# Performance work log

Measured on AMD Instinct MI355X. Metric: run time of the kernel, lower is better.

Reference implementation:

```python
import jax, jax.numpy as jnp
import numpy as np


def _round_ste(v):
    # straight-through rounding (typical LinearQuantize autograd STE)
    return v + jax.lax.stop_gradient(jnp.round(v) - v)


def setup_inputs() -> dict:
    key = jax.random.key(0)
    k1, k2, k3 = jax.random.split(key, 3)
    tokens, d_in, d_out = 8192, 2048, 2048
    x = jax.random.uniform(k1, (tokens, d_in), dtype=jnp.float32)  # non-negative acts
    weight = jax.random.normal(k2, (d_out, d_in), dtype=jnp.float32) * 0.02
    bias = jax.random.normal(k3, (d_out,), dtype=jnp.float32) * 0.02
    return {"x": x, "weight": weight, "bias": bias, "weight_bit": 8}


def reference(x, weight, bias, weight_bit):
    n = 2 ** weight_bit
    # stats computed on detached data (x.data/w.data in torch)
    wd = jax.lax.stop_gradient(weight)
    w_min = wd.min(axis=1)                      # [out]
    w_max = wd.max(axis=1)                      # [out]
    x_max = jax.lax.stop_gradient(x).max()
    scale_x = (n - 1) / jnp.clip(x_max, 1e-8)
    # activation quantization: round(scale_x * x - 0)
    q_x = _round_ste(scale_x * x)               # [T, in]
    # per-channel asymmetric weight quant (quantize_int)
    scale_w = (n - 1) / jnp.clip(w_max - w_min, 1e-8)   # [out]
    zp_w = scale_w * w_min                      # [out]
    q_w = _round_ste(scale_w[:, None] * weight - zp_w[:, None])  # [out, in]
    # bias quantized with combined scale, then clamped
    q_b = jnp.clip(_round_ste(bias * scale_w * scale_x), -n - 1, n)  # [out]
    # fake-int GEMM + zero-point correction + rescale
    mult = jnp.einsum('ti,oi->to', q_x, q_w) + q_b      # [T, out]
    res = mult + zp_w * q_x.sum(-1, keepdims=True)
    return res / scale_x / scale_w
```

## Files before the change

### kernel.cpp

```cpp
#include <hip/hip_runtime.h>
#include <stdint.h>

typedef __attribute__((ext_vector_type(4))) int i32x4;

__device__ inline float wave_max(float v){ for(int o=32;o;o>>=1) v=fmaxf(v,__shfl_xor(v,o)); return v; }
__device__ inline float wave_min(float v){ for(int o=32;o;o>>=1) v=fminf(v,__shfl_xor(v,o)); return v; }
__device__ inline int   wave_sum(int v){ for(int o=32;o;o>>=1) v+=__shfl_xor(v,o); return v; }

__device__ inline void gload16(const void* g, void* l){
  __builtin_amdgcn_global_load_lds((const __attribute__((address_space(1))) char*)g,
                                   (__attribute__((address_space(3))) char*)l, 16, 0, 0);
}

__global__ void k_xmax_partial(const float* __restrict__ x, long long n4,
                               float* __restrict__ partials){
  long long i = (long long)blockIdx.x*blockDim.x + threadIdx.x;
  long long stride = (long long)gridDim.x*blockDim.x;
  const float4* x4 = (const float4*)x;
  float m = 0.f;
  for(; i < n4; i += stride){
    float4 v = x4[i];
    m = fmaxf(m, fmaxf(fmaxf(v.x,v.y),fmaxf(v.z,v.w)));
  }
  m = wave_max(m);
  __shared__ float sm[4];
  int lane = threadIdx.x & 63, wid = threadIdx.x >> 6;
  if(lane==0) sm[wid] = m;
  __syncthreads();
  if(threadIdx.x==0)
    partials[blockIdx.x] = fmaxf(fmaxf(sm[0],sm[1]),fmaxf(sm[2],sm[3]));
}

__global__ void k_xmax_final(const float* __restrict__ partials, int nPart,
                             uint32_t* __restrict__ xmax_bits){
  float m = 0.f;
  for(int i = threadIdx.x; i < nPart; i += 256) m = fmaxf(m, partials[i]);
  m = wave_max(m);
  __shared__ float sm[4];
  int lane = threadIdx.x & 63, wid = threadIdx.x >> 6;
  if(lane==0) sm[wid] = m;
  __syncthreads();
  if(threadIdx.x==0)
    *xmax_bits = __float_as_uint(fmaxf(fmaxf(sm[0],sm[1]),fmaxf(sm[2],sm[3])));
}

__global__ void k_wstat(const float* __restrict__ w,
                        const int* __restrict__ wbit,
                        float* __restrict__ scale_w, float* __restrict__ zp_w,
                        float* __restrict__ winv,
                        int* __restrict__ cint, char* __restrict__ qw, int din){
  int row = blockIdx.x, tid = threadIdx.x;
  int lane = tid & 63, wid = tid >> 6;
  const float4* wr4 = (const float4*)(w + (long long)row*din);
  float4 a = wr4[tid*2], b = wr4[tid*2+1];
  float v[8] = {a.x,a.y,a.z,a.w,b.x,b.y,b.z,b.w};
  float mn = v[0], mx = v[0];
  for(int j=1;j<8;j++){ mn=fminf(mn,v[j]); mx=fmaxf(mx,v[j]); }
  float wmn = wave_min(mn), wmx = wave_max(mx);
  __shared__ float smn[4], smx[4];
  __shared__ float s_sw, s_zp;
  if(lane==0){ smn[wid]=wmn; smx[wid]=wmx; }
  __syncthreads();
  if(tid==0){
    float fmn = fminf(fminf(smn[0],smn[1]),fminf(smn[2],smn[3]));
    float fmx = fmaxf(fmaxf(smx[0],smx[1]),fmaxf(smx[2],smx[3]));
    int n = 1 << *wbit;
    float nm1 = (float)(n-1);
    float rngc = fmaxf(__fsub_rn(fmx, fmn), 1e-8f);
    float sw = __fdiv_rn(nm1, rngc);
    float zp = __fmul_rn(sw, fmn);
    s_sw = sw; s_zp = zp;
    scale_w[row] = sw; zp_w[row] = zp;
    winv[row] = __fdiv_rn(rngc, nm1);
  }
  __syncthreads();
  float sw = s_sw, zp = s_zp;
  int qsum = 0; uint32_t lo = 0, hi = 0;
  for(int j=0;j<8;j++){
    int q = (int)rintf(__fsub_rn(__fmul_rn(sw, v[j]), zp));
    qsum += q;
    uint32_t u = (uint32_t)((q - 128) & 0xff);
    if(j<4) lo |= u << (8*j); else hi |= u << (8*(j-4));
  }
  uint32_t* qrow = (uint32_t*)(qw + (long long)row*din);
  qrow[tid*2] = lo; qrow[tid*2+1] = hi;
  int wsum = wave_sum(qsum);
  __shared__ int ssum[4];
  if(lane==0) ssum[wid] = wsum;
  __syncthreads();
  if(tid==0){
    int Sb = ssum[0]+ssum[1]+ssum[2]+ssum[3];
    cint[row] = 128*Sb - 128*128*din;
  }
}

__global__ void k_xquant(const float* __restrict__ x, const int* __restrict__ wbit,
                         const uint32_t* __restrict__ xmax_bits,
                         char* __restrict__ qx, int* __restrict__ Sa, int din){
  int row = blockIdx.x, tid = threadIdx.x;
  int lane = tid & 63, wid = tid >> 6;
  int n = 1 << *wbit;
  float nm1 = (float)(n-1);
  float sx = __fdiv_rn(nm1, fmaxf(__uint_as_float(*xmax_bits), 1e-8f));
  const float4* xr4 = (const float4*)(x + (long long)row*din);
  float4 a = xr4[tid*2], b = xr4[tid*2+1];
  float v[8] = {a.x,a.y,a.z,a.w,b.x,b.y,b.z,b.w};
  int qsum = 0; uint32_t lo = 0, hi = 0;
  for(int j=0;j<8;j++){
    int q = (int)rintf(__fmul_rn(sx, v[j]));
    qsum += q;
    uint32_t u = (uint32_t)((q - 128) & 0xff);
    if(j<4) lo |= u << (8*j); else hi |= u << (8*(j-4));
  }
  uint32_t* qrow = (uint32_t*)(qx + (long long)row*din);
  qrow[tid*2] = lo; qrow[tid*2+1] = hi;
  int wsum = wave_sum(qsum);
  __shared__ int ssum[4];
  if(lane==0) ssum[wid] = wsum;
  __syncthreads();
  if(tid==0) Sa[row] = ssum[0]+ssum[1]+ssum[2]+ssum[3];
}

__global__ __launch_bounds__(512, 2) void k_gemm(
    const char* __restrict__ qx, const char* __restrict__ qw,
    const int* __restrict__ Sa, const int* __restrict__ cint,
    const float* __restrict__ scale_w, const float* __restrict__ winv,
    const float* __restrict__ zp_w, const float* __restrict__ bias,
    const int* __restrict__ wbit, const uint32_t* __restrict__ xmax_bits,
    float* __restrict__ out, int T, int dout, int din){
  extern __shared__ char lds[];
  const int tid = threadIdx.x, lane = tid & 63, wid = tid >> 6;
  const int wr = wid >> 2, wc = wid & 3;
  const int tileN = blockIdx.x, tileM = blockIdx.y;
  const int nt = din / 128;

  const int i0 = tid, i1 = tid + 512;
  const int r0 = i0 >> 2, r1 = i1 >> 2;
  const int sc0 = ((i0 & 3) ^ ((r0 >> 1) & 3)) * 16;
  const int sc1 = ((i1 & 3) ^ ((r1 >> 1) & 3)) * 16;
  const char* aS0 = qx + ((long long)tileM*256 + r0)*din + sc0;
  const char* aS1 = qx + ((long long)tileM*256 + r1)*din + sc1;
  const char* bS0 = qw + ((long long)tileN*256 + r0)*din + sc0;
  const char* bS1 = qw + ((long long)tileN*256 + r1)*din + sc1;
  const int d0 = i0*16, d1 = i1*16;

  const int physo = (((lane >> 4) ^ ((lane >> 1) & 3)) * 16);
  const int arowL = wr*128 + (lane & 15);
  const int browL = wc*64  + (lane & 15);

  i32x4 acc[8][4] = {};
  i32x4 af[4], bf[4];

#define STAGE_A(KS, KOFF, NB) do{ \
    gload16(aS0 + (KOFF) + (KS)*64, (NB) + (KS)*16384 + d0); \
    gload16(aS1 + (KOFF) + (KS)*64, (NB) + (KS)*16384 + d1); }while(0)
#define STAGE_B(KS, KOFF, NB) do{ \
    gload16(bS0 + (KOFF) + (KS)*64, (NB) + 32768 + (KS)*16384 + d0); \
    gload16(bS1 + (KOFF) + (KS)*64, (NB) + 32768 + (KS)*16384 + d1); }while(0)

  STAGE_A(0, 0, lds); STAGE_B(0, 0, lds);
  STAGE_A(1, 0, lds); STAGE_B(1, 0, lds);
  asm volatile("s_waitcnt vmcnt(4)" ::: "memory");
  __builtin_amdgcn_s_barrier();

  for(int t = 0; t < nt; ++t){
    char* Ab = lds + (t & 1)*65536;
    char* Bb = Ab + 32768;
    char* NB = lds + ((t & 1)^1)*65536;
    const bool ld = (t + 1 < nt);
    const int koff = (t + 1)*128;

#define PH(MH, KS, DO_B, STAGE_STMT, VM_STMT) do{ \
    if(DO_B){ _Pragma("unroll") \
      for(int ni=0;ni<4;++ni) bf[ni] = *(const i32x4*)(Bb + (KS)*16384 + (browL + ni*16)*64 + physo); } \
    _Pragma("unroll") \
    for(int mi=0;mi<4;++mi) af[mi] = *(const i32x4*)(Ab + (KS)*16384 + (arowL + (MH)*64 + mi*16)*64 + physo); \
    STAGE_STMT; \
    __builtin_amdgcn_s_barrier(); \
    __builtin_amdgcn_s_setprio(1); \
    _Pragma("unroll") \
    for(int mi=0;mi<4;++mi){ _Pragma("unroll") \
      for(int ni=0;ni<4;++ni) \
        acc[(MH)*4+mi][ni] = __builtin_amdgcn_mfma_i32_16x16x64_i8(af[mi], bf[ni], acc[(MH)*4+mi][ni], 0,0,0); } \
    __builtin_amdgcn_s_setprio(0); \
    VM_STMT; \
    __builtin_amdgcn_s_barrier(); }while(0)

    PH(0, 0, true,  if(ld) STAGE_A(0, koff, NB), );
    PH(1, 0, false, if(ld) STAGE_B(0, koff, NB),
       if(ld){ asm volatile("s_waitcnt vmcnt(4)" ::: "memory"); }
       else  { asm volatile("s_waitcnt vmcnt(0)" ::: "memory"); });
    PH(0, 1, true,  if(ld) STAGE_A(1, koff, NB), );
    PH(1, 1, false, if(ld) STAGE_B(1, koff, NB),
       if(ld){ asm volatile("s_waitcnt vmcnt(4)" ::: "memory"); });
#undef PH
  }

  const int n = 1 << *wbit;
  const float nm1 = (float)(n-1);
  const float xmaxc = fmaxf(__uint_as_float(*xmax_bits), 1e-8f);
  const float sx = __fdiv_rn(nm1, xmaxc);
  const float inv_sx = __fdiv_rn(xmaxc, nm1);
  const int colL = tileN*256 + wc*64 + (lane & 15);
  const int rowL = tileM*256 + wr*128 + ((lane >> 4) * 4);
  float invc[4], zp4[4]; int ci4[4];
  #pragma unroll
  for(int ni=0; ni<4; ++ni){
    int o = colL + ni*16;
    float sw = scale_w[o];
    float qbf = rintf(__fmul_rn(__fmul_rn(bias[o], sw), sx));
    qbf = fminf(fmaxf(qbf, -(float)(n+1)), (float)n);
    ci4[ni] = cint[o] + (int)qbf;
    invc[ni] = __fmul_rn(winv[o], inv_sx);
    zp4[ni]  = zp_w[o];
  }
  #pragma unroll
  for(int mi=0; mi<8; ++mi){
    int rb = rowL + mi*16;
    int sav[4];
    #pragma unroll
    for(int r=0; r<4; ++r) sav[r] = Sa[rb + r];
    #pragma unroll
    for(int ni=0; ni<4; ++ni){
      #pragma unroll
      for(int r=0; r<4; ++r){
        int iv = acc[mi][ni][r] + 128*sav[r] + ci4[ni];
        float f = (float)iv + zp4[ni]*(float)sav[r];
        out[(long long)(rb + r)*dout + colL + ni*16] = __fmul_rn(f, invc[ni]);
      }
    }
  }
}

extern "C" void kernel_launch(void* const* d_in, const int* in_sizes, int n_in,
                              void* d_out, int out_size, void* d_ws, size_t ws_size,
                              hipStream_t stream){
  const float* x    = (const float*)d_in[0];
  const float* w    = (const float*)d_in[1];
  const float* bias = (const float*)d_in[2];
  const int*   wbit = (const int*)d_in[3];
  int dout = in_sizes[2];
  int din  = in_sizes[1] / dout;
  int T    = in_sizes[0] / din;

  const int NPART = 2048;
  char* ws = (char*)d_ws;
  uint32_t* xmax_bits = (uint32_t*)ws;
  size_t off = 256;
  float* partials = (float*)(ws + off); off += 4*(size_t)NPART;
  float* scale_w = (float*)(ws + off); off += 4*(size_t)dout;
  float* zp_w    = (float*)(ws + off); off += 4*(size_t)dout;
  float* winv    = (float*)(ws + off); off += 4*(size_t)dout;
  int*   cint    = (int*)(ws + off);   off += 4*(size_t)dout;
  int*   Sa      = (int*)(ws + off);   off += 4*(size_t)T;
  off = (off + 255) & ~(size_t)255;
  char*  qw      = ws + off;           off += (size_t)dout*din;
  char*  qx      = ws + off;           off += (size_t)T*din;

  long long n4 = (long long)T*din/4;
  k_xmax_partial<<<NPART, 256, 0, stream>>>(x, n4, partials);
  k_xmax_final<<<1, 256, 0, stream>>>(partials, NPART, xmax_bits);
  k_wstat<<<dout, 256, 0, stream>>>(w, wbit, scale_w, zp_w, winv, cint, qw, din);
  k_xquant<<<T, 256, 0, stream>>>(x, wbit, xmax_bits, qx, Sa, din);
  dim3 grid(dout/256, T/256);
  k_gemm<<<grid, 512, 131072, stream>>>(qx, qw, Sa, cint, scale_w, winv, zp_w, bias,
                                        wbit, xmax_bits, (float*)d_out, T, dout, din);
}
```

Baseline: 80.34 us.

## Drop xmax final kernel and stage GEMM epilogue through LDS for coalesced stores

Removes the single-block xmax reduction kernel; every k_xquant and k_gemm block now re-reduces the 2048 partial maxima itself, which removes one launch and a serialized tiny kernel at the cost of redundant reads. The GEMM epilogue now writes each 16-row slice of results into LDS and then writes it out as row-contiguous float4 stores instead of scattered scalar stores, aiming for better write coalescing. This adds extra barriers per slice in the epilogue.

```diff
diff --git a/kernel.cpp b/kernel.cpp
--- a/kernel.cpp
+++ b/kernel.cpp
@@ -29,19 +29,6 @@
   __syncthreads();
   if(threadIdx.x==0)
     partials[blockIdx.x] = fmaxf(fmaxf(sm[0],sm[1]),fmaxf(sm[2],sm[3]));
-}
-
-__global__ void k_xmax_final(const float* __restrict__ partials, int nPart,
-                             uint32_t* __restrict__ xmax_bits){
-  float m = 0.f;
-  for(int i = threadIdx.x; i < nPart; i += 256) m = fmaxf(m, partials[i]);
-  m = wave_max(m);
-  __shared__ float sm[4];
-  int lane = threadIdx.x & 63, wid = threadIdx.x >> 6;
-  if(lane==0) sm[wid] = m;
-  __syncthreads();
-  if(threadIdx.x==0)
-    *xmax_bits = __float_as_uint(fmaxf(fmaxf(sm[0],sm[1]),fmaxf(sm[2],sm[3])));
 }
 
 __global__ void k_wstat(const float* __restrict__ w,
@@ -95,13 +82,20 @@
 }
 
 __global__ void k_xquant(const float* __restrict__ x, const int* __restrict__ wbit,
-                         const uint32_t* __restrict__ xmax_bits,
+                         const float* __restrict__ partials, int nPart,
                          char* __restrict__ qx, int* __restrict__ Sa, int din){
   int row = blockIdx.x, tid = threadIdx.x;
   int lane = tid & 63, wid = tid >> 6;
+  float mm = 0.f;
+  for(int i=tid;i<nPart;i+=256) mm = fmaxf(mm, partials[i]);
+  mm = wave_max(mm);
+  __shared__ float sm[4];
+  if(lane==0) sm[wid] = mm;
+  __syncthreads();
+  const float xmax = fmaxf(fmaxf(sm[0],sm[1]),fmaxf(sm[2],sm[3]));
   int n = 1 << *wbit;
   float nm1 = (float)(n-1);
-  float sx = __fdiv_rn(nm1, fmaxf(__uint_as_float(*xmax_bits), 1e-8f));
+  float sx = __fdiv_rn(nm1, fmaxf(xmax, 1e-8f));
   const float4* xr4 = (const float4*)(x + (long long)row*din);
   float4 a = xr4[tid*2], b = xr4[tid*2+1];
   float v[8] = {a.x,a.y,a.z,a.w,b.x,b.y,b.z,b.w};
@@ -126,7 +120,7 @@
     const int* __restrict__ Sa, const int* __restrict__ cint,
     const float* __restrict__ scale_w, const float* __restrict__ winv,
     const float* __restrict__ zp_w, const float* __restrict__ bias,
-    const int* __restrict__ wbit, const uint32_t* __restrict__ xmax_bits,
+    const int* __restrict__ wbit, const float* __restrict__ partials, int nPart,
     float* __restrict__ out, int T, int dout, int din){
   extern __shared__ char lds[];
   const int tid = threadIdx.x, lane = tid & 63, wid = tid >> 6;
@@ -196,9 +190,21 @@
 #undef PH
   }
 
+  __syncthreads();
+  {
+    float mm = 0.f;
+    for(int i = tid; i < nPart; i += 512) mm = fmaxf(mm, partials[i]);
+    mm = wave_max(mm);
+    if(lane==0) ((float*)lds)[wid] = mm;
+  }
+  __syncthreads();
+  float xmax = 0.f;
+  #pragma unroll
+  for(int i=0;i<8;i++) xmax = fmaxf(xmax, ((float*)lds)[i]);
+
   const int n = 1 << *wbit;
   const float nm1 = (float)(n-1);
-  const float xmaxc = fmaxf(__uint_as_float(*xmax_bits), 1e-8f);
+  const float xmaxc = fmaxf(xmax, 1e-8f);
   const float sx = __fdiv_rn(nm1, xmaxc);
   const float inv_sx = __fdiv_rn(xmaxc, nm1);
   const int colL = tileN*256 + wc*64 + (lane & 15);
@@ -214,20 +220,34 @@
     invc[ni] = __fmul_rn(winv[o], inv_sx);
     zp4[ni]  = zp_w[o];
   }
+
+  float* ebuf = (float*)lds;
+  const int lwr  = wr*16 + ((lane >> 4) * 4);
+  const int lcol = wc*64 + (lane & 15);
   #pragma unroll
   for(int mi=0; mi<8; ++mi){
     int rb = rowL + mi*16;
     int sav[4];
     #pragma unroll
     for(int r=0; r<4; ++r) sav[r] = Sa[rb + r];
+    __syncthreads();
     #pragma unroll
     for(int ni=0; ni<4; ++ni){
       #pragma unroll
       for(int r=0; r<4; ++r){
         int iv = acc[mi][ni][r] + 128*sav[r] + ci4[ni];
         float f = (float)iv + zp4[ni]*(float)sav[r];
-        out[(long long)(rb + r)*dout + colL + ni*16] = __fmul_rn(f, invc[ni]);
+        ebuf[(lwr + r)*256 + lcol + ni*16] = __fmul_rn(f, invc[ni]);
       }
+    }
+    __syncthreads();
+    #pragma unroll
+    for(int p=0; p<4; ++p){
+      int idx = tid + p*512;
+      int lr = idx >> 6, cc = (idx & 63)*4;
+      float4 v = *(const float4*)&ebuf[lr*256 + cc];
+      int gr = tileM*256 + (lr>>4)*128 + mi*16 + (lr&15);
+      *(float4*)&out[(long long)gr*dout + tileN*256 + cc] = v;
     }
   }
 }
@@ -245,7 +265,6 @@
 
   const int NPART = 2048;
   char* ws = (char*)d_ws;
-  uint32_t* xmax_bits = (uint32_t*)ws;
   size_t off = 256;
   float* partials = (float*)(ws + off); off += 4*(size_t)NPART;
   float* scale_w = (float*)(ws + off); off += 4*(size_t)dout;
@@ -259,10 +278,9 @@
 
   long long n4 = (long long)T*din/4;
   k_xmax_partial<<<NPART, 256, 0, stream>>>(x, n4, partials);
-  k_xmax_final<<<1, 256, 0, stream>>>(partials, NPART, xmax_bits);
+  k_xquant<<<T, 256, 0, stream>>>(x, wbit, partials, NPART, qx, Sa, din);
   k_wstat<<<dout, 256, 0, stream>>>(w, wbit, scale_w, zp_w, winv, cint, qw, din);
-  k_xquant<<<T, 256, 0, stream>>>(x, wbit, xmax_bits, qx, Sa, din);
   dim3 grid(dout/256, T/256);
   k_gemm<<<grid, 512, 131072, stream>>>(qx, qw, Sa, cint, scale_w, winv, zp_w, bias,
-                                        wbit, xmax_bits, (float*)d_out, T, dout, din);
-}
+                                        wbit, partials, NPART, (float*)d_out, T, dout, din);
+}
```

Result: slower. 83.12 us (+3.5%).
